# Optimization experiments

Hardware: AMD Instinct MI355X
Metric: run time of the kernel (lower is better)

## Reference

```python
import jax, jax.numpy as jnp
import numpy as np

B, N, DIM = 4, 2048, 256
K = 16            # num_nearest_neighbors
EDGE_DIM = 2
M_DIM = 64
EIN = 2 * DIM + 1 + EDGE_DIM   # 515, edge_mlp input dim
VALID_RADIUS = 0.0
MASK_FILL = 1e5


def setup_inputs() -> dict:
    key = jax.random.key(0)
    ks = jax.random.split(key, 16)
    emb = jax.random.normal(ks[0], (B, N, DIM), dtype=jnp.float32)
    coors = jax.random.normal(ks[1], (B, N, 3), dtype=jnp.float32)
    adj = jax.random.bernoulli(ks[2], 0.004, (B, N, N))            # avg degree ~8
    feat = jax.random.normal(ks[3], (B, N, N, EDGE_DIM), dtype=jnp.float32)
    mask = jax.random.bernoulli(ks[4], 0.9, (B, N))
    s = 0.02
    eW1 = jax.random.normal(ks[5], (EIN, 2 * EIN), dtype=jnp.float32) * s
    eb1 = jnp.zeros((2 * EIN,), dtype=jnp.float32)
    eW2 = jax.random.normal(ks[6], (2 * EIN, M_DIM), dtype=jnp.float32) * s
    eb2 = jnp.zeros((M_DIM,), dtype=jnp.float32)
    nW1 = jax.random.normal(ks[7], (DIM + M_DIM, 2 * DIM), dtype=jnp.float32) * s
    nb1 = jnp.zeros((2 * DIM,), dtype=jnp.float32)
    nW2 = jax.random.normal(ks[8], (2 * DIM, DIM), dtype=jnp.float32) * s
    nb2 = jnp.zeros((DIM,), dtype=jnp.float32)
    return {"emb": emb, "coors": coors, "adj": adj, "feat": feat, "mask": mask,
            "eW1": eW1, "eb1": eb1, "eW2": eW2, "eb2": eb2,
            "nW1": nW1, "nb1": nb1, "nW2": nW2, "nb2": nb2}


def reference(emb, coors, adj, feat, mask, eW1, eb1, eW2, eb2, nW1, nb1, nW2, nb2):
    b, n, d = emb.shape
    # pairwise squared distances [b,n,n]
    rel = coors[:, :, None, :] - coors[:, None, :, :]
    rel_dist = jnp.sum(rel * rel, axis=-1)
    # ranking for kNN selection (masked pairs pushed far, self=-1, adjacent=0)
    rank_mask = mask[:, :, None] & mask[:, None, :]
    ranking = jnp.where(rank_mask, rel_dist, MASK_FILL)
    eye = jnp.eye(n, dtype=bool)[None]
    adj_ns = adj & ~eye
    ranking = jnp.where(eye, -1.0, ranking)
    ranking = jnp.where(adj_ns, 0.0, ranking)
    # k smallest
    neg_vals, idx = jax.lax.top_k(-ranking, K)          # idx [b,n,K]
    nbhd_ranking = -neg_vals
    nbhd_mask = nbhd_ranking <= VALID_RADIUS
    # gathers
    rel_dist_k = jnp.take_along_axis(rel_dist, idx, axis=2)[..., None]      # [b,n,K,1]
    edges_k = jnp.take_along_axis(feat, idx[..., None], axis=2)             # [b,n,K,E]
    feats_j = jax.vmap(lambda f, ix: f[ix])(emb, idx)                       # [b,n,K,d]
    feats_i = jnp.broadcast_to(emb[:, :, None, :], feats_j.shape)
    edge_input = jnp.concatenate([feats_i, feats_j, rel_dist_k, edges_k], axis=-1)
    # edge MLP: Linear -> SiLU -> Linear -> SiLU (dropout=0 in eval)
    h = jax.nn.silu(edge_input @ eW1 + eb1)
    m_ij = jax.nn.silu(h @ eW2 + eb2)                                       # [b,n,K,m]
    # pair mask
    mask_j = jax.vmap(lambda m, ix: m[ix])(mask, idx)                       # [b,n,K]
    pair_mask = (mask[:, :, None] & mask_j) & nbhd_mask
    m_ij = jnp.where(pair_mask[..., None], m_ij, 0.0)
    m_i = jnp.sum(m_ij, axis=2)                                             # [b,n,m]
    # node MLP with residual (norm_feats=False)
    node_in = jnp.concatenate([emb, m_i], axis=-1)
    node_out = jax.nn.silu(node_in @ nW1 + nb1) @ nW2 + nb2 + emb
    # update_coors=False -> coors unchanged; module returns full tuple
    return (node_out, coors, adj, feat, mask)
```

## Files before the change

### kernel.cpp

```cpp
#include <hip/hip_runtime.h>
#include <stdint.h>

typedef unsigned short ushort_t;

#define NN    2048
#define DIMC  256
#define H1    1030
#define MD    64
#define NROWS 8192

#define HP       1040

#define KPAD     1056
#define NKS      33

#define NPQ      2060
#define NPQP     2112
#define KN1      320
#define KN2      512

#define ADJ_BLKS 2048
#define PREP_TOT (NPQP*DIMC + 512*KN1 + 256*KN2 + MD*KPAD + 3*HP + NROWS*DIMC)
#define MACCZ    (NROWS*MD/4)
#define COORSZ   (24576/4)
#define N2_BLKS  256
#define FCOPY4   (33554432/4)

typedef __bf16 bf16x8 __attribute__((ext_vector_type(8)));
typedef float  f32x4  __attribute__((ext_vector_type(4)));
typedef ushort_t u16x8 __attribute__((ext_vector_type(8)));

__device__ __forceinline__ float bfu2f(ushort_t u){ union{unsigned u; float f;} v; v.u = ((unsigned)u)<<16; return v.f; }
__device__ __forceinline__ ushort_t f2bfu(float f){ union{float f; unsigned u;} v; v.f=f; unsigned r = (v.u + 0x7FFFu + ((v.u>>16)&1u))>>16; return (ushort_t)r; }
__device__ __forceinline__ float siluf(float x){ return x / (1.0f + __expf(-x)); }
__device__ __forceinline__ void split_hilo(float v, ushort_t& hi, ushort_t& lo){
    hi = f2bfu(v);
    lo = f2bfu(v - bfu2f(hi));
}

__global__ void stage1(const int* __restrict__ adj, const int* __restrict__ mask,
                       const float* __restrict__ coors,
                       const float* __restrict__ eW1, const float* __restrict__ nW1,
                       const float* __restrict__ nW2, const float* __restrict__ eW2,
                       const float* __restrict__ emb,
                       float* __restrict__ out_adj, float* __restrict__ out_mask,
                       float* __restrict__ out_coors,
                       int* __restrict__ pairs, int* __restrict__ counter,
                       ushort_t* __restrict__ Wpq_h, ushort_t* __restrict__ Wpq_l,
                       ushort_t* __restrict__ W1T_h, ushort_t* __restrict__ W1T_l,
                       ushort_t* __restrict__ NW2T_h, ushort_t* __restrict__ NW2T_l,
                       ushort_t* __restrict__ W2T, float* __restrict__ wt4,
                       ushort_t* __restrict__ Ah, ushort_t* __restrict__ Al,
                       float* __restrict__ macc)
{
    if (blockIdx.x < ADJ_BLKS) {
        const int w = threadIdx.x >> 6, lane = threadIdx.x & 63;
        const int row = blockIdx.x*4 + w;
        const int b = row >> 11, i = row & (NN-1);
        __shared__ int nbrs[4][15];
        int total = 0;
        const size_t rbase = (size_t)row * NN;
        const int4* arow = (const int4*)(adj + rbase);
        float4* orow = (float4*)(out_adj + rbase);
        for (int c = 0; c < NN/256; c++) {
            int4 v = arow[c*64 + lane];
            int j0 = c*256 + lane*4;
            float4 ov; ov.x = v.x?1.f:0.f; ov.y = v.y?1.f:0.f; ov.z = v.z?1.f:0.f; ov.w = v.w?1.f:0.f;
            orow[c*64 + lane] = ov;
            bool p0 = v.x && (j0   != i);
            bool p1 = v.y && (j0+1 != i);
            bool p2 = v.z && (j0+2 != i);
            bool p3 = v.w && (j0+3 != i);
            unsigned long long b0 = __ballot(p0), b1 = __ballot(p1), b2 = __ballot(p2), b3 = __ballot(p3);
            unsigned long long below = (1ull<<lane)-1ull;
            int slot = total + __popcll(b0&below)+__popcll(b1&below)+__popcll(b2&below)+__popcll(b3&below);
            if (p0 && slot < 15) nbrs[w][slot] = j0;
            slot += p0;
            if (p1 && slot < 15) nbrs[w][slot] = j0+1;
            slot += p1;
            if (p2 && slot < 15) nbrs[w][slot] = j0+2;
            slot += p2;
            if (p3 && slot < 15) nbrs[w][slot] = j0+3;
            total += __popcll(b0)+__popcll(b1)+__popcll(b2)+__popcll(b3);
        }
        int cnt = total < 15 ? total : 15;
        const int mv = mask[row];
        if (lane == 0) out_mask[row] = mv ? 1.0f : 0.0f;
        if (mv != 0) {
            int jl = (lane < cnt) ? nbrs[w][lane] : 0;
            bool ok = (lane < cnt) && (mask[b*NN + jl] != 0);
            unsigned long long bm = __ballot(ok);
            int npair = 1 + __popcll(bm);
            int basep = 0;
            if (lane == 0) basep = atomicAdd(counter, npair);
            basep = __shfl(basep, 0);
            if (lane == 0) pairs[basep] = (row << 16) | i;
            if (ok) {
                int pos = basep + 1 + __popcll(bm & ((1ull<<lane)-1ull));
                pairs[pos] = (row << 16) | jl;
            }
        }
        return;
    }
    int t = (blockIdx.x - ADJ_BLKS)*256 + threadIdx.x;
    if (t < NPQP*DIMC) {
        int n = t >> 8, k = t & 255;
        float v = 0.f;
        if (n < H1) v = eW1[(size_t)k*H1 + n];
        else if (n < NPQ) v = eW1[(size_t)(256+k)*H1 + (n - H1)];
        ushort_t hi, lo; split_hilo(v, hi, lo);
        Wpq_h[t] = hi; Wpq_l[t] = lo;
        return;
    }
    t -= NPQP*DIMC;
    if (t < 512*KN1) {
        int n = t / KN1, k = t - n*KN1;
        ushort_t hi, lo; split_hilo(nW1[(size_t)k*512 + n], hi, lo);
        W1T_h[t] = hi; W1T_l[t] = lo;
        return;
    }
    t -= 512*KN1;
    if (t < 256*KN2) {
        int n = t >> 9, k = t & 511;
        ushort_t hi, lo; split_hilo(nW2[(size_t)k*256 + n], hi, lo);
        NW2T_h[t] = hi; NW2T_l[t] = lo;
        return;
    }
    t -= 256*KN2;
    if (t < MD*KPAD) {
        int n = t / KPAD, k = t - n*KPAD;
        W2T[t] = f2bfu((k < H1) ? eW2[(size_t)k*MD + n] : 0.0f);
        return;
    }
    t -= MD*KPAD;
    if (t < 3*HP) {
        int c = t / HP, k = t - c*HP;
        wt4[t] = (k < H1) ? eW1[(size_t)(512+c)*H1 + k] : 0.f;
        return;
    }
    t -= 3*HP;
    if (t < NROWS*DIMC) {
        int r = t >> 8, k = t & 255;
        ushort_t hi, lo; split_hilo(emb[t], hi, lo);
        Ah[(size_t)r*KN1 + k] = hi; Al[(size_t)r*KN1 + k] = lo;
        return;
    }
    t -= NROWS*DIMC;
    if (t < MACCZ) {
        float4 z; z.x = z.y = z.z = z.w = 0.f;
        ((float4*)macc)[t] = z;
        return;
    }
    t -= MACCZ;
    if (t < COORSZ) {
        ((float4*)out_coors)[t] = ((const float4*)coors)[t];
    }
}

template<int K>
__device__ __forceinline__ void mfma_tile2(const ushort_t* __restrict__ Ah, const ushort_t* __restrict__ Al, int sA,
                                           const ushort_t* __restrict__ Bh, const ushort_t* __restrict__ Bl, int sB,
                                           int lane, f32x4 (&acc)[2][4])
{
    const int m16 = lane & 15, kg = lane >> 4;
    const ushort_t* a0h = Ah + (size_t)m16*sA + kg*8;
    const ushort_t* a0l = Al + (size_t)m16*sA + kg*8;
    const ushort_t* a1h = a0h + (size_t)16*sA;
    const ushort_t* a1l = a0l + (size_t)16*sA;
    const ushort_t* brh = Bh + (size_t)m16*sB + kg*8;
    const ushort_t* brl = Bl + (size_t)m16*sB + kg*8;
#pragma unroll 4
    for (int ks = 0; ks < K/32; ks++) {
        bf16x8 a0h_ = *reinterpret_cast<const bf16x8*>(a0h + ks*32);
        bf16x8 a0l_ = *reinterpret_cast<const bf16x8*>(a0l + ks*32);
        bf16x8 a1h_ = *reinterpret_cast<const bf16x8*>(a1h + ks*32);
        bf16x8 a1l_ = *reinterpret_cast<const bf16x8*>(a1l + ks*32);
#pragma unroll
        for (int nf = 0; nf < 4; nf++) {
            bf16x8 bh = *reinterpret_cast<const bf16x8*>(brh + (size_t)(nf*16)*sB + ks*32);
            bf16x8 bl = *reinterpret_cast<const bf16x8*>(brl + (size_t)(nf*16)*sB + ks*32);
            acc[0][nf] = __builtin_amdgcn_mfma_f32_16x16x32_bf16(a0h_, bh, acc[0][nf], 0, 0, 0);
            acc[0][nf] = __builtin_amdgcn_mfma_f32_16x16x32_bf16(a0h_, bl, acc[0][nf], 0, 0, 0);
            acc[0][nf] = __builtin_amdgcn_mfma_f32_16x16x32_bf16(a0l_, bh, acc[0][nf], 0, 0, 0);
            acc[1][nf] = __builtin_amdgcn_mfma_f32_16x16x32_bf16(a1h_, bh, acc[1][nf], 0, 0, 0);
            acc[1][nf] = __builtin_amdgcn_mfma_f32_16x16x32_bf16(a1h_, bl, acc[1][nf], 0, 0, 0);
            acc[1][nf] = __builtin_amdgcn_mfma_f32_16x16x32_bf16(a1l_, bh, acc[1][nf], 0, 0, 0);
        }
    }
}

__global__ __launch_bounds__(256)
void gemm_pq_mfma(const ushort_t* __restrict__ Aeph, const ushort_t* __restrict__ Aepl,
                  const ushort_t* __restrict__ Wh, const ushort_t* __restrict__ Wl,
                  const float* __restrict__ eb1,
                  ushort_t* __restrict__ Pb, ushort_t* __restrict__ Qb)
{
    const int lane = threadIdx.x & 63, w = threadIdx.x >> 6;
    const int rowBase = blockIdx.x*128 + w*32;
    const int colBase = blockIdx.y*64;
    f32x4 acc[2][4] = {{{0,0,0,0},{0,0,0,0},{0,0,0,0},{0,0,0,0}},
                       {{0,0,0,0},{0,0,0,0},{0,0,0,0},{0,0,0,0}}};
    mfma_tile2<DIMC>(Aeph + (size_t)rowBase*KN1, Aepl + (size_t)rowBase*KN1, KN1,
                     Wh + (size_t)colBase*DIMC, Wl + (size_t)colBase*DIMC, DIMC, lane, acc);
    const int m16 = lane & 15, kg = lane >> 4;
#pragma unroll
    for (int tt = 0; tt < 2; tt++) {
#pragma unroll
        for (int nf = 0; nf < 4; nf++) {
#pragma unroll
            for (int r = 0; r < 4; r++) {
                int row = rowBase + tt*16 + kg*4 + r;
                int n = colBase + nf*16 + m16;
                if (n < H1) {
                    Pb[(size_t)row*HP + n] = f2bfu(acc[tt][nf][r] + eb1[n]);
                } else if (n < NPQ) {
                    Qb[(size_t)row*HP + (n - H1)] = f2bfu(acc[tt][nf][r]);
                }
            }
        }
    }
}

__global__ __launch_bounds__(256)
void node1_mfma(const ushort_t* __restrict__ Aeph, const ushort_t* __restrict__ Aepl,
                const ushort_t* __restrict__ W1h, const ushort_t* __restrict__ W1l,
                const float* __restrict__ macc,
                const float* __restrict__ nb1, ushort_t* __restrict__ Hh, ushort_t* __restrict__ Hl)
{
    const int lane = threadIdx.x & 63, w = threadIdx.x >> 6;
    const int rowBase = blockIdx.x*128 + w*32;
    const int colBase = blockIdx.y*64;
    f32x4 acc[2][4] = {{{0,0,0,0},{0,0,0,0},{0,0,0,0},{0,0,0,0}},
                       {{0,0,0,0},{0,0,0,0},{0,0,0,0},{0,0,0,0}}};
    mfma_tile2<DIMC>(Aeph + (size_t)rowBase*KN1, Aepl + (size_t)rowBase*KN1, KN1,
                     W1h + (size_t)colBase*KN1, W1l + (size_t)colBase*KN1, KN1, lane, acc);
    const int m16 = lane & 15, kg = lane >> 4;
    {
        const float* mr0 = macc + (size_t)(rowBase + m16)*MD;
        const float* mr1 = macc + (size_t)(rowBase + 16 + m16)*MD;
        const ushort_t* brh_b = W1h + ((size_t)colBase + m16)*KN1 + DIMC + kg*8;
        const ushort_t* brl_b = W1l + ((size_t)colBase + m16)*KN1 + DIMC + kg*8;
#pragma unroll
        for (int ks = 0; ks < 2; ks++) {
            int kk = ks*32 + kg*8;
            f32x4 va = *reinterpret_cast<const f32x4*>(mr0 + kk);
            f32x4 vb = *reinterpret_cast<const f32x4*>(mr0 + kk + 4);
            f32x4 vc = *reinterpret_cast<const f32x4*>(mr1 + kk);
            f32x4 vd = *reinterpret_cast<const f32x4*>(mr1 + kk + 4);
            u16x8 h0, l0, h1, l1;
#pragma unroll
            for (int e = 0; e < 8; e++) {
                ushort_t hi, lo;
                split_hilo((e < 4) ? va[e] : vb[e-4], hi, lo); h0[e] = hi; l0[e] = lo;
                split_hilo((e < 4) ? vc[e] : vd[e-4], hi, lo); h1[e] = hi; l1[e] = lo;
            }
            bf16x8 a0h = *reinterpret_cast<bf16x8*>(&h0);
            bf16x8 a0l = *reinterpret_cast<bf16x8*>(&l0);
            bf16x8 a1h = *reinterpret_cast<bf16x8*>(&h1);
            bf16x8 a1l = *reinterpret_cast<bf16x8*>(&l1);
#pragma unroll
            for (int nf = 0; nf < 4; nf++) {
                bf16x8 bh = *reinterpret_cast<const bf16x8*>(brh_b + (size_t)(nf*16)*KN1 + ks*32);
                bf16x8 bl = *reinterpret_cast<const bf16x8*>(brl_b + (size_t)(nf*16)*KN1 + ks*32);
                acc[0][nf] = __builtin_amdgcn_mfma_f32_16x16x32_bf16(a0h, bh, acc[0][nf], 0, 0, 0);
                acc[0][nf] = __builtin_amdgcn_mfma_f32_16x16x32_bf16(a0h, bl, acc[0][nf], 0, 0, 0);
                acc[0][nf] = __builtin_amdgcn_mfma_f32_16x16x32_bf16(a0l, bh, acc[0][nf], 0, 0, 0);
                acc[1][nf] = __builtin_amdgcn_mfma_f32_16x16x32_bf16(a1h, bh, acc[1][nf], 0, 0, 0);
                acc[1][nf] = __builtin_amdgcn_mfma_f32_16x16x32_bf16(a1h, bl, acc[1][nf], 0, 0, 0);
                acc[1][nf] = __builtin_amdgcn_mfma_f32_16x16x32_bf16(a1l, bh, acc[1][nf], 0, 0, 0);
            }
        }
    }
#pragma unroll
    for (int tt = 0; tt < 2; tt++) {
#pragma unroll
        for (int nf = 0; nf < 4; nf++) {
#pragma unroll
            for (int r = 0; r < 4; r++) {
                int row = rowBase + tt*16 + kg*4 + r;
                int col = colBase + nf*16 + m16;
                float s = siluf(acc[tt][nf][r] + nb1[col]);
                ushort_t hi, lo; split_hilo(s, hi, lo);
                Hh[(size_t)row*KN2 + col] = hi;
                Hl[(size_t)row*KN2 + col] = lo;
            }
        }
    }
}

__global__ __launch_bounds__(256)
void stage5(const ushort_t* __restrict__ Hh, const ushort_t* __restrict__ Hl,
            const ushort_t* __restrict__ W2h, const ushort_t* __restrict__ W2l,
            const float* __restrict__ nb2, const float* __restrict__ emb,
            const float* __restrict__ feat,
            float* __restrict__ out_node, float* __restrict__ out_feat)
{
    if (blockIdx.x >= N2_BLKS) {
        int t = (blockIdx.x - N2_BLKS)*256 + threadIdx.x;
        if (t < FCOPY4) ((float4*)out_feat)[t] = ((const float4*)feat)[t];
        return;
    }
    const int rb = blockIdx.x & 63, cb = blockIdx.x >> 6;
    const int lane = threadIdx.x & 63, w = threadIdx.x >> 6;
    const int rowBase = rb*128 + w*32;
    const int colBase = cb*64;
    f32x4 acc[2][4] = {{{0,0,0,0},{0,0,0,0},{0,0,0,0},{0,0,0,0}},
                       {{0,0,0,0},{0,0,0,0},{0,0,0,0},{0,0,0,0}}};
    mfma_tile2<KN2>(Hh + (size_t)rowBase*KN2, Hl + (size_t)rowBase*KN2, KN2,
                    W2h + (size_t)colBase*KN2, W2l + (size_t)colBase*KN2, KN2, lane, acc);
    const int m16 = lane & 15, kg = lane >> 4;
#pragma unroll
    for (int tt = 0; tt < 2; tt++) {
#pragma unroll
        for (int nf = 0; nf < 4; nf++) {
#pragma unroll
            for (int r = 0; r < 4; r++) {
                int row = rowBase + tt*16 + kg*4 + r;
                int col = colBase + nf*16 + m16;
                size_t o = (size_t)row*DIMC + col;
                out_node[o] = acc[tt][nf][r] + nb2[col] + emb[o];
            }
        }
    }
}

__global__ __launch_bounds__(256)
void edge_mfma(const int* __restrict__ pairs, const int* __restrict__ counter,
               const ushort_t* __restrict__ P, const ushort_t* __restrict__ Q,
               const float* __restrict__ coors, const float* __restrict__ feat,
               const float* __restrict__ wt4,
               const ushort_t* __restrict__ W2T, const float* __restrict__ eb2,
               float* __restrict__ macc)
{
    const int np = counter[0];
    const int lane = threadIdx.x & 63;
    const int w = threadIdx.x >> 6;
    const int wbase = blockIdx.x*64 + w*16;
    if (wbase >= np) return;
    const int m16 = lane & 15, kg = lane >> 4;

    const int pidx = wbase + m16;
    const int e = pairs[(pidx < np) ? pidx : wbase];
    const int row = e >> 16, j = e & 0xFFFF;
    const int jr = ((row >> 11) << 11) + j;
    const float dx = coors[row*3+0] - coors[jr*3+0];
    const float dy = coors[row*3+1] - coors[jr*3+1];
    const float dz = coors[row*3+2] - coors[jr*3+2];
    const float d  = dx*dx + dy*dy + dz*dz;
    const size_t fo = ((size_t)row*NN + j)*2;
    const float f0 = feat[fo], f1 = feat[fo+1];
    const ushort_t* Prow = P + (size_t)row*HP;
    const ushort_t* Qrow = Q + (size_t)jr*HP;
    const float* w512 = wt4;
    const float* w513 = wt4 + HP;
    const float* w514 = wt4 + 2*HP;
    const int kb = kg*8;

    f32x4 acc[4] = {{0,0,0,0},{0,0,0,0},{0,0,0,0},{0,0,0,0}};

    for (int ks = 0; ks < NKS; ks++) {
        const int k0 = ks*32 + kb;
        u16x8 hv = {0,0,0,0,0,0,0,0};
        u16x8 lv = {0,0,0,0,0,0,0,0};
        if (k0 < H1) {
            u16x8 pv8 = *reinterpret_cast<const u16x8*>(Prow + k0);
            u16x8 qv8 = *reinterpret_cast<const u16x8*>(Qrow + k0);
            f32x4 wa0 = *reinterpret_cast<const f32x4*>(w512 + k0);
            f32x4 wa1 = *reinterpret_cast<const f32x4*>(w512 + k0 + 4);
            f32x4 wb0 = *reinterpret_cast<const f32x4*>(w513 + k0);
            f32x4 wb1 = *reinterpret_cast<const f32x4*>(w513 + k0 + 4);
            f32x4 wc0 = *reinterpret_cast<const f32x4*>(w514 + k0);
            f32x4 wc1 = *reinterpret_cast<const f32x4*>(w514 + k0 + 4);
#pragma unroll
            for (int ee = 0; ee < 8; ee++) {
                float va = (ee < 4) ? wa0[ee] : wa1[ee-4];
                float vb = (ee < 4) ? wb0[ee] : wb1[ee-4];
                float vc = (ee < 4) ? wc0[ee] : wc1[ee-4];
                float x = bfu2f(pv8[ee]) + bfu2f(qv8[ee]) + d*va + f0*vb + f1*vc;
                float h = (k0 + ee < H1) ? siluf(x) : 0.f;
                union {float f; unsigned u;} cv; cv.f = h;
                unsigned hib = cv.u & 0xFFFF0000u;
                hv[ee] = (ushort_t)(hib >> 16);
                union {unsigned u; float f;} hf; hf.u = hib;
                union {float f; unsigned u;} lw; lw.f = h - hf.f;
                lv[ee] = (ushort_t)(lw.u >> 16);
            }
        }
        bf16x8 ah = *reinterpret_cast<bf16x8*>(&hv);
        bf16x8 al = *reinterpret_cast<bf16x8*>(&lv);
        const ushort_t* Wk = W2T + k0;
#pragma unroll
        for (int nf = 0; nf < 4; nf++) {
            bf16x8 bfr = *reinterpret_cast<const bf16x8*>(Wk + (size_t)(nf*16 + m16)*KPAD);
            acc[nf] = __builtin_amdgcn_mfma_f32_16x16x32_bf16(ah, bfr, acc[nf], 0, 0, 0);
            acc[nf] = __builtin_amdgcn_mfma_f32_16x16x32_bf16(al, bfr, acc[nf], 0, 0, 0);
        }
    }

#pragma unroll
    for (int nf = 0; nf < 4; nf++) {
        const int n = nf*16 + m16;
        const float bias = eb2[n];
#pragma unroll
        for (int r = 0; r < 4; r++) {
            int pe = wbase + kg*4 + r;
            if (pe < np) {
                int rr = pairs[pe] >> 16;
                float m = siluf(acc[nf][r] + bias);
                atomicAdd(&macc[(size_t)rr*MD + n], m);
            }
        }
    }
}

extern "C" void kernel_launch(void* const* d_in, const int* in_sizes, int n_in,
                              void* d_out, int out_size, void* d_ws, size_t ws_size,
                              hipStream_t stream)
{
    const float* emb   = (const float*)d_in[0];
    const float* coors = (const float*)d_in[1];
    const int*   adj   = (const int*)d_in[2];
    const float* feat  = (const float*)d_in[3];
    const int*   mask  = (const int*)d_in[4];
    const float* eW1   = (const float*)d_in[5];
    const float* eb1   = (const float*)d_in[6];
    const float* eW2   = (const float*)d_in[7];
    const float* eb2   = (const float*)d_in[8];
    const float* nW1   = (const float*)d_in[9];
    const float* nb1   = (const float*)d_in[10];
    const float* nW2   = (const float*)d_in[11];
    const float* nb2   = (const float*)d_in[12];

    float* out       = (float*)d_out;
    float* out_node  = out;
    float* out_coors = out + 2097152;
    float* out_adj   = out + 2121728;
    float* out_feat  = out + 18898944;
    float* out_mask  = out + 52453376;

    char* ws = (char*)d_ws;
    int*      counter = (int*)(ws + 0);
    float*    macc    = (float*)(ws + 256);
    int*      pairs   = (int*)(ws + 2097408);
    ushort_t* Pbuf    = (ushort_t*)(ws + 2621696);
    float*    wt4     = (float*)(ws + 19661056);
    ushort_t* Hid_h   = (ushort_t*)(ws + 19673536);
    ushort_t* Hid_l   = (ushort_t*)(ws + 28062144);
    ushort_t* NW2T_h  = (ushort_t*)(ws + 36450752);
    ushort_t* NW2T_l  = (ushort_t*)(ws + 36712896);

    char* scr = (char*)out_feat;
    ushort_t* Aep_h = (ushort_t*)(scr + 0);
    ushort_t* Aep_l = (ushort_t*)(scr + 5242880);
    ushort_t* Wpq_h = (ushort_t*)(scr + 10485760);
    ushort_t* Wpq_l = (ushort_t*)(scr + 11567104);
    ushort_t* W1T_h = (ushort_t*)(scr + 12648448);
    ushort_t* W1T_l = (ushort_t*)(scr + 12976128);
    ushort_t* Qbuf  = (ushort_t*)(scr + 13303808);

    ushort_t* W2T = (ushort_t*)out_node;

    hipMemsetAsync(counter, 0, 256, stream);

    {
        int extra = (PREP_TOT + MACCZ + COORSZ + 255)/256;
        stage1<<<ADJ_BLKS + extra, 256, 0, stream>>>(adj, mask, coors, eW1, nW1, nW2, eW2, emb,
                                                     out_adj, out_mask, out_coors, pairs, counter,
                                                     Wpq_h, Wpq_l, W1T_h, W1T_l, NW2T_h, NW2T_l,
                                                     W2T, wt4, Aep_h, Aep_l, macc);
    }

    gemm_pq_mfma<<<dim3(NROWS/128, NPQP/64), 256, 0, stream>>>(Aep_h, Aep_l, Wpq_h, Wpq_l, eb1, Pbuf, Qbuf);

    edge_mfma<<<2048, 256, 0, stream>>>(pairs, counter, Pbuf, Qbuf, coors, feat,
                                        wt4, W2T, eb2, macc);

    node1_mfma<<<dim3(NROWS/128, 512/64), 256, 0, stream>>>(Aep_h, Aep_l, W1T_h, W1T_l, macc, nb1, Hid_h, Hid_l);

    stage5<<<N2_BLKS + FCOPY4/256, 256, 0, stream>>>(Hid_h, Hid_l, NW2T_h, NW2T_l, nb2, emb, feat,
                                                     out_node, out_feat);
}
```

Measured before the change: 698.4 us.

## Fuse node MLP layers into one kernel with hidden activations in LDS

Merges the two node MLP GEMM kernels into a single kernel where each block computes 32 rows of the SiLU hidden layer, stores it as split bf16 in shared memory, then runs the second GEMM plus bias and residual. This removes the global write and reread of the hidden buffer and one launch. Aep and W1T buffers move into workspace because the feat copy now runs concurrently in the same kernel and would clobber the scratch in out_feat. Tradeoff is fewer, heavier blocks (256) with large LDS usage and repeated weight reads per block.

Result: no change. 704.9 us (+0.9%).

```diff
diff --git a/kernel.cpp b/kernel.cpp
--- a/kernel.cpp
+++ b/kernel.cpp
@@ -23,7 +23,7 @@
 #define PREP_TOT (NPQP*DIMC + 512*KN1 + 256*KN2 + MD*KPAD + 3*HP + NROWS*DIMC)
 #define MACCZ    (NROWS*MD/4)
 #define COORSZ   (24576/4)
-#define N2_BLKS  256
+#define N4_BLKS  256
 #define FCOPY4   (33554432/4)
 
 typedef __bf16 bf16x8 __attribute__((ext_vector_type(8)));
@@ -222,109 +222,6 @@
 }
 
 __global__ __launch_bounds__(256)
-void node1_mfma(const ushort_t* __restrict__ Aeph, const ushort_t* __restrict__ Aepl,
-                const ushort_t* __restrict__ W1h, const ushort_t* __restrict__ W1l,
-                const float* __restrict__ macc,
-                const float* __restrict__ nb1, ushort_t* __restrict__ Hh, ushort_t* __restrict__ Hl)
-{
-    const int lane = threadIdx.x & 63, w = threadIdx.x >> 6;
-    const int rowBase = blockIdx.x*128 + w*32;
-    const int colBase = blockIdx.y*64;
-    f32x4 acc[2][4] = {{{0,0,0,0},{0,0,0,0},{0,0,0,0},{0,0,0,0}},
-                       {{0,0,0,0},{0,0,0,0},{0,0,0,0},{0,0,0,0}}};
-    mfma_tile2<DIMC>(Aeph + (size_t)rowBase*KN1, Aepl + (size_t)rowBase*KN1, KN1,
-                     W1h + (size_t)colBase*KN1, W1l + (size_t)colBase*KN1, KN1, lane, acc);
-    const int m16 = lane & 15, kg = lane >> 4;
-    {
-        const float* mr0 = macc + (size_t)(rowBase + m16)*MD;
-        const float* mr1 = macc + (size_t)(rowBase + 16 + m16)*MD;
-        const ushort_t* brh_b = W1h + ((size_t)colBase + m16)*KN1 + DIMC + kg*8;
-        const ushort_t* brl_b = W1l + ((size_t)colBase + m16)*KN1 + DIMC + kg*8;
-#pragma unroll
-        for (int ks = 0; ks < 2; ks++) {
-            int kk = ks*32 + kg*8;
-            f32x4 va = *reinterpret_cast<const f32x4*>(mr0 + kk);
-            f32x4 vb = *reinterpret_cast<const f32x4*>(mr0 + kk + 4);
-            f32x4 vc = *reinterpret_cast<const f32x4*>(mr1 + kk);
-            f32x4 vd = *reinterpret_cast<const f32x4*>(mr1 + kk + 4);
-            u16x8 h0, l0, h1, l1;
-#pragma unroll
-            for (int e = 0; e < 8; e++) {
-                ushort_t hi, lo;
-                split_hilo((e < 4) ? va[e] : vb[e-4], hi, lo); h0[e] = hi; l0[e] = lo;
-                split_hilo((e < 4) ? vc[e] : vd[e-4], hi, lo); h1[e] = hi; l1[e] = lo;
-            }
-            bf16x8 a0h = *reinterpret_cast<bf16x8*>(&h0);
-            bf16x8 a0l = *reinterpret_cast<bf16x8*>(&l0);
-            bf16x8 a1h = *reinterpret_cast<bf16x8*>(&h1);
-            bf16x8 a1l = *reinterpret_cast<bf16x8*>(&l1);
-#pragma unroll
-            for (int nf = 0; nf < 4; nf++) {
-                bf16x8 bh = *reinterpret_cast<const bf16x8*>(brh_b + (size_t)(nf*16)*KN1 + ks*32);
-                bf16x8 bl = *reinterpret_cast<const bf16x8*>(brl_b + (size_t)(nf*16)*KN1 + ks*32);
-                acc[0][nf] = __builtin_amdgcn_mfma_f32_16x16x32_bf16(a0h, bh, acc[0][nf], 0, 0, 0);
-                acc[0][nf] = __builtin_amdgcn_mfma_f32_16x16x32_bf16(a0h, bl, acc[0][nf], 0, 0, 0);
-                acc[0][nf] = __builtin_amdgcn_mfma_f32_16x16x32_bf16(a0l, bh, acc[0][nf], 0, 0, 0);
-                acc[1][nf] = __builtin_amdgcn_mfma_f32_16x16x32_bf16(a1h, bh, acc[1][nf], 0, 0, 0);
-                acc[1][nf] = __builtin_amdgcn_mfma_f32_16x16x32_bf16(a1h, bl, acc[1][nf], 0, 0, 0);
-                acc[1][nf] = __builtin_amdgcn_mfma_f32_16x16x32_bf16(a1l, bh, acc[1][nf], 0, 0, 0);
-            }
-        }
-    }
-#pragma unroll
-    for (int tt = 0; tt < 2; tt++) {
-#pragma unroll
-        for (int nf = 0; nf < 4; nf++) {
-#pragma unroll
-            for (int r = 0; r < 4; r++) {
-                int row = rowBase + tt*16 + kg*4 + r;
-                int col = colBase + nf*16 + m16;
-                float s = siluf(acc[tt][nf][r] + nb1[col]);
-                ushort_t hi, lo; split_hilo(s, hi, lo);
-                Hh[(size_t)row*KN2 + col] = hi;
-                Hl[(size_t)row*KN2 + col] = lo;
-            }
-        }
-    }
-}
-
-__global__ __launch_bounds__(256)
-void stage5(const ushort_t* __restrict__ Hh, const ushort_t* __restrict__ Hl,
-            const ushort_t* __restrict__ W2h, const ushort_t* __restrict__ W2l,
-            const float* __restrict__ nb2, const float* __restrict__ emb,
-            const float* __restrict__ feat,
-            float* __restrict__ out_node, float* __restrict__ out_feat)
-{
-    if (blockIdx.x >= N2_BLKS) {
-        int t = (blockIdx.x - N2_BLKS)*256 + threadIdx.x;
-        if (t < FCOPY4) ((float4*)out_feat)[t] = ((const float4*)feat)[t];
-        return;
-    }
-    const int rb = blockIdx.x & 63, cb = blockIdx.x >> 6;
-    const int lane = threadIdx.x & 63, w = threadIdx.x >> 6;
-    const int rowBase = rb*128 + w*32;
-    const int colBase = cb*64;
-    f32x4 acc[2][4] = {{{0,0,0,0},{0,0,0,0},{0,0,0,0},{0,0,0,0}},
-                       {{0,0,0,0},{0,0,0,0},{0,0,0,0},{0,0,0,0}}};
-    mfma_tile2<KN2>(Hh + (size_t)rowBase*KN2, Hl + (size_t)rowBase*KN2, KN2,
-                    W2h + (size_t)colBase*KN2, W2l + (size_t)colBase*KN2, KN2, lane, acc);
-    const int m16 = lane & 15, kg = lane >> 4;
-#pragma unroll
-    for (int tt = 0; tt < 2; tt++) {
-#pragma unroll
-        for (int nf = 0; nf < 4; nf++) {
-#pragma unroll
-            for (int r = 0; r < 4; r++) {
-                int row = rowBase + tt*16 + kg*4 + r;
-                int col = colBase + nf*16 + m16;
-                size_t o = (size_t)row*DIMC + col;
-                out_node[o] = acc[tt][nf][r] + nb2[col] + emb[o];
-            }
-        }
-    }
-}
-
-__global__ __launch_bounds__(256)
 void edge_mfma(const int* __restrict__ pairs, const int* __restrict__ counter,
                const ushort_t* __restrict__ P, const ushort_t* __restrict__ Q,
                const float* __restrict__ coors, const float* __restrict__ feat,
@@ -413,6 +310,126 @@
     }
 }
 
+__global__ __launch_bounds__(256)
+void stage4(const ushort_t* __restrict__ Aeph, const ushort_t* __restrict__ Aepl,
+            const ushort_t* __restrict__ W1h, const ushort_t* __restrict__ W1l,
+            const float* __restrict__ macc, const float* __restrict__ nb1,
+            const ushort_t* __restrict__ W2h, const ushort_t* __restrict__ W2l,
+            const float* __restrict__ nb2, const float* __restrict__ emb,
+            const float* __restrict__ feat,
+            float* __restrict__ out_node, float* __restrict__ out_feat)
+{
+    if (blockIdx.x >= N4_BLKS) {
+        int t = (blockIdx.x - N4_BLKS)*256 + threadIdx.x;
+        if (t < FCOPY4) ((float4*)out_feat)[t] = ((const float4*)feat)[t];
+        return;
+    }
+    __shared__ ushort_t hidh[32][520];
+    __shared__ ushort_t hidl[32][520];
+    const int lane = threadIdx.x & 63, w = threadIdx.x >> 6;
+    const int m16 = lane & 15, kg = lane >> 4;
+    const int rowBase = blockIdx.x * 32;
+
+#pragma unroll
+    for (int ct = 0; ct < 2; ct++) {
+        const int colBase = w*128 + ct*64;
+        f32x4 acc[2][4] = {{{0,0,0,0},{0,0,0,0},{0,0,0,0},{0,0,0,0}},
+                           {{0,0,0,0},{0,0,0,0},{0,0,0,0},{0,0,0,0}}};
+        mfma_tile2<DIMC>(Aeph + (size_t)rowBase*KN1, Aepl + (size_t)rowBase*KN1, KN1,
+                         W1h + (size_t)colBase*KN1, W1l + (size_t)colBase*KN1, KN1, lane, acc);
+        {
+            const float* mr0 = macc + (size_t)(rowBase + m16)*MD;
+            const float* mr1 = macc + (size_t)(rowBase + 16 + m16)*MD;
+            const ushort_t* brh_b = W1h + ((size_t)colBase + m16)*KN1 + DIMC + kg*8;
+            const ushort_t* brl_b = W1l + ((size_t)colBase + m16)*KN1 + DIMC + kg*8;
+#pragma unroll
+            for (int ks = 0; ks < 2; ks++) {
+                int kk = ks*32 + kg*8;
+                f32x4 va = *reinterpret_cast<const f32x4*>(mr0 + kk);
+                f32x4 vb = *reinterpret_cast<const f32x4*>(mr0 + kk + 4);
+                f32x4 vc = *reinterpret_cast<const f32x4*>(mr1 + kk);
+                f32x4 vd = *reinterpret_cast<const f32x4*>(mr1 + kk + 4);
+                u16x8 h0, l0, h1, l1;
+#pragma unroll
+                for (int e = 0; e < 8; e++) {
+                    ushort_t hi, lo;
+                    split_hilo((e < 4) ? va[e] : vb[e-4], hi, lo); h0[e] = hi; l0[e] = lo;
+                    split_hilo((e < 4) ? vc[e] : vd[e-4], hi, lo); h1[e] = hi; l1[e] = lo;
+                }
+                bf16x8 a0h = *reinterpret_cast<bf16x8*>(&h0);
+                bf16x8 a0l = *reinterpret_cast<bf16x8*>(&l0);
+                bf16x8 a1h = *reinterpret_cast<bf16x8*>(&h1);
+                bf16x8 a1l = *reinterpret_cast<bf16x8*>(&l1);
+#pragma unroll
+                for (int nf = 0; nf < 4; nf++) {
+                    bf16x8 bh = *reinterpret_cast<const bf16x8*>(brh_b + (size_t)(nf*16)*KN1 + ks*32);
+                    bf16x8 bl = *reinterpret_cast<const bf16x8*>(brl_b + (size_t)(nf*16)*KN1 + ks*32);
+                    acc[0][nf] = __builtin_amdgcn_mfma_f32_16x16x32_bf16(a0h, bh, acc[0][nf], 0, 0, 0);
+                    acc[0][nf] = __builtin_amdgcn_mfma_f32_16x16x32_bf16(a0h, bl, acc[0][nf], 0, 0, 0);
+                    acc[0][nf] = __builtin_amdgcn_mfma_f32_16x16x32_bf16(a0l, bh, acc[0][nf], 0, 0, 0);
+                    acc[1][nf] = __builtin_amdgcn_mfma_f32_16x16x32_bf16(a1h, bh, acc[1][nf], 0, 0, 0);
+                    acc[1][nf] = __builtin_amdgcn_mfma_f32_16x16x32_bf16(a1h, bl, acc[1][nf], 0, 0, 0);
+                    acc[1][nf] = __builtin_amdgcn_mfma_f32_16x16x32_bf16(a1l, bh, acc[1][nf], 0, 0, 0);
+                }
+            }
+        }
+#pragma unroll
+        for (int tt = 0; tt < 2; tt++) {
+#pragma unroll
+            for (int nf = 0; nf < 4; nf++) {
+#pragma unroll
+                for (int r = 0; r < 4; r++) {
+                    int lrow = tt*16 + kg*4 + r;
+                    int col = colBase + nf*16 + m16;
+                    float s = siluf(acc[tt][nf][r] + nb1[col]);
+                    ushort_t hi, lo; split_hilo(s, hi, lo);
+                    hidh[lrow][col] = hi;
+                    hidl[lrow][col] = lo;
+                }
+            }
+        }
+    }
+    __syncthreads();
+
+    f32x4 acc2[2][4] = {{{0,0,0,0},{0,0,0,0},{0,0,0,0},{0,0,0,0}},
+                        {{0,0,0,0},{0,0,0,0},{0,0,0,0},{0,0,0,0}}};
+    const int colB2 = w*64;
+    const ushort_t* b2h = W2h + ((size_t)colB2 + m16)*KN2 + kg*8;
+    const ushort_t* b2l = W2l + ((size_t)colB2 + m16)*KN2 + kg*8;
+#pragma unroll 4
+    for (int ks = 0; ks < KN2/32; ks++) {
+        const int k = ks*32 + kg*8;
+        bf16x8 a0h = *reinterpret_cast<const bf16x8*>(&hidh[m16][k]);
+        bf16x8 a0l = *reinterpret_cast<const bf16x8*>(&hidl[m16][k]);
+        bf16x8 a1h = *reinterpret_cast<const bf16x8*>(&hidh[m16+16][k]);
+        bf16x8 a1l = *reinterpret_cast<const bf16x8*>(&hidl[m16+16][k]);
+#pragma unroll
+        for (int nf = 0; nf < 4; nf++) {
+            bf16x8 bh = *reinterpret_cast<const bf16x8*>(b2h + (size_t)(nf*16)*KN2 + ks*32);
+            bf16x8 bl = *reinterpret_cast<const bf16x8*>(b2l + (size_t)(nf*16)*KN2 + ks*32);
+            acc2[0][nf] = __builtin_amdgcn_mfma_f32_16x16x32_bf16(a0h, bh, acc2[0][nf], 0, 0, 0);
+            acc2[0][nf] = __builtin_amdgcn_mfma_f32_16x16x32_bf16(a0h, bl, acc2[0][nf], 0, 0, 0);
+            acc2[0][nf] = __builtin_amdgcn_mfma_f32_16x16x32_bf16(a0l, bh, acc2[0][nf], 0, 0, 0);
+            acc2[1][nf] = __builtin_amdgcn_mfma_f32_16x16x32_bf16(a1h, bh, acc2[1][nf], 0, 0, 0);
+            acc2[1][nf] = __builtin_amdgcn_mfma_f32_16x16x32_bf16(a1h, bl, acc2[1][nf], 0, 0, 0);
+            acc2[1][nf] = __builtin_amdgcn_mfma_f32_16x16x32_bf16(a1l, bh, acc2[1][nf], 0, 0, 0);
+        }
+    }
+#pragma unroll
+    for (int tt = 0; tt < 2; tt++) {
+#pragma unroll
+        for (int nf = 0; nf < 4; nf++) {
+#pragma unroll
+            for (int r = 0; r < 4; r++) {
+                int row = rowBase + tt*16 + kg*4 + r;
+                int col = colB2 + nf*16 + m16;
+                size_t o = (size_t)row*DIMC + col;
+                out_node[o] = acc2[tt][nf][r] + nb2[col] + emb[o];
+            }
+        }
+    }
+}
+
 extern "C" void kernel_launch(void* const* d_in, const int* in_sizes, int n_in,
                               void* d_out, int out_size, void* d_ws, size_t ws_size,
                               hipStream_t stream)
@@ -444,19 +461,17 @@
     int*      pairs   = (int*)(ws + 2097408);
     ushort_t* Pbuf    = (ushort_t*)(ws + 2621696);
     float*    wt4     = (float*)(ws + 19661056);
-    ushort_t* Hid_h   = (ushort_t*)(ws + 19673536);
-    ushort_t* Hid_l   = (ushort_t*)(ws + 28062144);
-    ushort_t* NW2T_h  = (ushort_t*)(ws + 36450752);
-    ushort_t* NW2T_l  = (ushort_t*)(ws + 36712896);
+    ushort_t* NW2T_h  = (ushort_t*)(ws + 19673536);
+    ushort_t* NW2T_l  = (ushort_t*)(ws + 19935680);
+    ushort_t* Aep_h   = (ushort_t*)(ws + 20197824);
+    ushort_t* Aep_l   = (ushort_t*)(ws + 25440704);
+    ushort_t* W1T_h   = (ushort_t*)(ws + 30683584);
+    ushort_t* W1T_l   = (ushort_t*)(ws + 31011264);
 
     char* scr = (char*)out_feat;
-    ushort_t* Aep_h = (ushort_t*)(scr + 0);
-    ushort_t* Aep_l = (ushort_t*)(scr + 5242880);
-    ushort_t* Wpq_h = (ushort_t*)(scr + 10485760);
-    ushort_t* Wpq_l = (ushort_t*)(scr + 11567104);
-    ushort_t* W1T_h = (ushort_t*)(scr + 12648448);
-    ushort_t* W1T_l = (ushort_t*)(scr + 12976128);
-    ushort_t* Qbuf  = (ushort_t*)(scr + 13303808);
+    ushort_t* Wpq_h = (ushort_t*)(scr + 0);
+    ushort_t* Wpq_l = (ushort_t*)(scr + 1081344);
+    ushort_t* Qbuf  = (ushort_t*)(scr + 2162688);
 
     ushort_t* W2T = (ushort_t*)out_node;
 
@@ -475,8 +490,7 @@
     edge_mfma<<<2048, 256, 0, stream>>>(pairs, counter, Pbuf, Qbuf, coors, feat,
                                         wt4, W2T, eb2, macc);
 
-    node1_mfma<<<dim3(NROWS/128, 512/64), 256, 0, stream>>>(Aep_h, Aep_l, W1T_h, W1T_l, macc, nb1, Hid_h, Hid_l);
-
-    stage5<<<N2_BLKS + FCOPY4/256, 256, 0, stream>>>(Hid_h, Hid_l, NW2T_h, NW2T_l, nb2, emb, feat,
+    stage4<<<N4_BLKS + FCOPY4/256, 256, 0, stream>>>(Aep_h, Aep_l, W1T_h, W1T_l, macc, nb1,
+                                                     NW2T_h, NW2T_l, nb2, emb, feat,
                                                      out_node, out_feat);
 }
```
